# Kernel tuning notes

Measured on AMD Instinct MI355X. Metric: run time of the kernel, lower is better.

## Reference

```python
import jax, jax.numpy as jnp
import numpy as np

# DeformConv (v1, mmcv-style) config
N, C, H, W = 4, 64, 128, 128
OUT_C, KH, KW = 64, 3, 3
STRIDE, PAD, DIL, DG = 1, 1, 1, 1  # groups = 1


def setup_inputs() -> dict:
    key = jax.random.key(0)
    k1, k2, k3 = jax.random.split(key, 3)
    x = jax.random.normal(k1, (N, C, H, W), dtype=jnp.float32)
    offset = jax.random.normal(k2, (N, 2 * DG * KH * KW, H, W), dtype=jnp.float32)
    n_fan = C * KH * KW
    std = 1.0 / np.sqrt(n_fan)
    weight = jax.random.uniform(k3, (OUT_C, C, KH, KW), minval=-std, maxval=std, dtype=jnp.float32)
    return {"input_tensor": x, "offset": offset, "weight": weight}


def _deform_conv(x, offset, weight, stride, padding, dilation, dg):
    n, c, h, w = x.shape
    o, cin_g, kh, kw = weight.shape
    k = kh * kw
    ho = (h + 2 * padding - dilation * (kh - 1) - 1) // stride + 1
    wo = (w + 2 * padding - dilation * (kw - 1) - 1) // stride + 1

    # offset layout: [n, dg*k*2, ho, wo] with (dy, dx) pairs per kernel point
    off = offset.reshape(n, dg, k, 2, ho, wo)
    dy, dx = off[:, :, :, 0], off[:, :, :, 1]  # [n, dg, k, ho, wo]

    ky, kx = jnp.meshgrid(jnp.arange(kh), jnp.arange(kw), indexing="ij")
    ky = ky.reshape(k).astype(x.dtype)
    kx = kx.reshape(k).astype(x.dtype)

    base_y = (jnp.arange(ho) * stride - padding).astype(x.dtype)
    base_x = (jnp.arange(wo) * stride - padding).astype(x.dtype)
    # sampling positions [n, dg, k, ho, wo]
    py = base_y[None, None, None, :, None] + (ky * dilation)[None, None, :, None, None] + dy
    px = base_x[None, None, None, None, :] + (kx * dilation)[None, None, :, None, None] + dx

    cg = c // dg
    xg = x.reshape(n, dg, cg, h * w)

    y0 = jnp.floor(py)
    x0 = jnp.floor(px)
    ly = py - y0  # bilinear weights
    lx = px - x0
    y0i = y0.astype(jnp.int32)
    x0i = x0.astype(jnp.int32)

    def gather(yi, xi):
        # zero contribution for out-of-bounds neighbors (matches mmcv bilinear)
        valid = (yi >= 0) & (yi < h) & (xi >= 0) & (xi < w)
        idx = jnp.clip(yi, 0, h - 1) * w + jnp.clip(xi, 0, w - 1)  # [n, dg, k, ho, wo]
        v = jnp.take_along_axis(xg, idx.reshape(n, dg, 1, -1), axis=3)  # [n, dg, cg, k*ho*wo]
        v = v.reshape(n, dg, cg, k, ho, wo)
        return v * valid[:, :, None].astype(x.dtype)

    v00 = gather(y0i, x0i)
    v01 = gather(y0i, x0i + 1)
    v10 = gather(y0i + 1, x0i)
    v11 = gather(y0i + 1, x0i + 1)

    wy = ly[:, :, None]  # [n, dg, 1, k, ho, wo]
    wx = lx[:, :, None]
    sampled = (v00 * (1 - wy) * (1 - wx) + v01 * (1 - wy) * wx
               + v10 * wy * (1 - wx) + v11 * wy * wx)
    sampled = sampled.reshape(n, c, k, ho, wo)  # dg*cg == c, groups == 1

    return jnp.einsum("nckhw,ock->nohw", sampled, weight.reshape(o, cin_g, k))


def reference(input_tensor, offset, weight):
    return _deform_conv(input_tensor, offset, weight, STRIDE, PAD, DIL, DG)
```

## Files before the change

### kernel.cpp

```cpp
#include <hip/hip_runtime.h>

#define HW 16384
#define CIN 64
#define COUT 64
#define HH 128
#define WW 128
#define NB 4
#define PXB 32
#define TPB 4

typedef __attribute__((ext_vector_type(8))) short bf16x8;
typedef __attribute__((ext_vector_type(4))) float f32x4;
typedef __attribute__((ext_vector_type(8))) unsigned short u16x8;

__device__ __forceinline__ unsigned short f32_bf16(float f) {
  unsigned u = __builtin_bit_cast(unsigned, f);
  u += 0x7fffu + ((u >> 16) & 1u);
  return (unsigned short)(u >> 16);
}
__device__ __forceinline__ float bits_f32(unsigned u) {
  return __builtin_bit_cast(float, u);
}

#define SYNCB()                                              \
  do {                                                       \
    asm volatile("s_waitcnt lgkmcnt(0)" ::: "memory");       \
    __builtin_amdgcn_s_barrier();                            \
    __builtin_amdgcn_sched_barrier(0);                       \
  } while (0)

__global__ __launch_bounds__(256) void prep_kernel(
    const float* __restrict__ x, const float* __restrict__ w,
    unsigned short* __restrict__ xt, unsigned short* __restrict__ wt) {
  __shared__ float tile[64][65];
  const int bid = blockIdx.x;
  if (bid < 1024) {
    const int n = bid >> 8;
    const int hw0 = (bid & 255) * 64;
    const int tx = threadIdx.x & 63;
    const int ty = threadIdx.x >> 6;
    const float* xp = x + (size_t)n * CIN * HW;
    #pragma unroll
    for (int c = ty; c < 64; c += 4)
      tile[c][tx] = xp[(size_t)c * HW + hw0 + tx];
    __syncthreads();
    unsigned short* xtp = xt + (size_t)n * HW * CIN;
    #pragma unroll
    for (int hw = ty; hw < 64; hw += 4)
      xtp[(size_t)(hw0 + hw) * CIN + tx] = f32_bf16(tile[tx][hw]);
  } else {
    const int i = (bid - 1024) * 256 + threadIdx.x;
    if (i < 64 * 576) {
      const int o = i / 576;
      const int t = i % 576;
      const int c = t & 63;
      const int k = t >> 6;
      wt[i] = f32_bf16(w[((size_t)o * 64 + c) * 9 + k]);
    }
  }
}

__global__ __launch_bounds__(256, 2) void deform_mfma(
    const unsigned short* __restrict__ xt, const float* __restrict__ offset,
    const unsigned short* __restrict__ wt, float* __restrict__ out) {
  __shared__ unsigned short s[PXB][584];
  __shared__ f32x4 pw[288];
  __shared__ uint2 pidx[288];
  const int tid = threadIdx.x;
  const int wave = tid >> 6;
  const int lane = tid & 63;
  const int g16 = lane >> 4;
  const int li16 = lane & 15;
  const int px = wave * 8 + (lane >> 3);
  const int li8 = lane & 7;
  const int base = blockIdx.x * (PXB * TPB);
  const int n = base >> 14;
  const int rem_base = base & 16383;

  const float* offb = offset + (size_t)n * 18 * HW;
  const unsigned short* xli = xt + (size_t)n * HW * CIN + li8 * 8;

  const int px0 = tid & 31;
  const int tap0 = tid >> 5;

  bf16x8 bv[18];
  {
    const unsigned short* bp = wt + ((size_t)(wave * 16 + li16)) * 576 + g16 * 8;
    #pragma unroll
    for (int i = 0; i < 18; ++i)
      bv[i] = *(const bf16x8*)(bp + i * 32);
  }

  #define PARAMS(tt, tapv, dyv, dxv)                                       \
    do {                                                                   \
      const int rem = rem_base + (tt) * PXB + px0;                         \
      const int y = rem >> 7;                                              \
      const int x = rem & 127;                                             \
      const float fy = floorf(dyv);                                        \
      const float fx = floorf(dxv);                                        \
      const float ly = (dyv)-fy;                                           \
      const float lx = (dxv)-fx;                                           \
      const int y0 = y - 1 + ((tapv) / 3) + (int)fy;                       \
      const int x0 = x - 1 + ((tapv) % 3) + (int)fx;                       \
      const int y1 = y0 + 1, x1 = x0 + 1;                                  \
      const bool vy0 = (unsigned)y0 < (unsigned)HH;                        \
      const bool vy1 = (unsigned)y1 < (unsigned)HH;                        \
      const bool vx0 = (unsigned)x0 < (unsigned)WW;                        \
      const bool vx1 = (unsigned)x1 < (unsigned)WW;                        \
      const int cy0 = min(max(y0, 0), HH - 1);                             \
      const int cy1 = min(max(y1, 0), HH - 1);                             \
      const int cx0 = min(max(x0, 0), WW - 1);                             \
      const int cx1 = min(max(x1, 0), WW - 1);                             \
      const float omly = 1.f - ly, omlx = 1.f - lx;                        \
      f32x4 w4;                                                            \
      w4[0] = (vy0 && vx0) ? omly * omlx : 0.f;                            \
      w4[1] = (vy0 && vx1) ? omly * lx : 0.f;                              \
      w4[2] = (vy1 && vx0) ? ly * omlx : 0.f;                              \
      w4[3] = (vy1 && vx1) ? ly * lx : 0.f;                                \
      const unsigned i00 = (unsigned)(cy0 * WW + cx0);                     \
      const unsigned i01 = (unsigned)(cy0 * WW + cx1);                     \
      const unsigned i10 = (unsigned)(cy1 * WW + cx0);                     \
      const unsigned i11 = (unsigned)(cy1 * WW + cx1);                     \
      pw[(tapv)*32 + px0] = w4;                                            \
      pidx[(tapv)*32 + px0] = make_uint2(i00 | (i01 << 16), i10 | (i11 << 16)); \
    } while (0)

  u16x8 V[3][4];

  #define ISSUE(kk, sl)                                                    \
    do {                                                                   \
      const uint2 id = pidx[(kk)*32 + px];                                 \
      V[sl][0] = *(const u16x8*)(xli + (size_t)(id.x & 0xffffu) * CIN);    \
      V[sl][1] = *(const u16x8*)(xli + (size_t)(id.x >> 16) * CIN);        \
      V[sl][2] = *(const u16x8*)(xli + (size_t)(id.y & 0xffffu) * CIN);    \
      V[sl][3] = *(const u16x8*)(xli + (size_t)(id.y >> 16) * CIN);        \
    } while (0)

  #define BLEND(kk, sl)                                                    \
    do {                                                                   \
      const f32x4 w = pw[(kk)*32 + px];                                    \
      float a[8] = {0.f, 0.f, 0.f, 0.f, 0.f, 0.f, 0.f, 0.f};               \
      _Pragma("unroll")                                                    \
      for (int c = 0; c < 4; ++c) {                                        \
        _Pragma("unroll")                                                  \
        for (int j = 0; j < 8; ++j)                                        \
          a[j] = fmaf(bits_f32((unsigned)V[sl][c][j] << 16), w[c], a[j]);  \
      }                                                                    \
      unsigned r0, r1, r2, r3;                                             \
      asm("v_cvt_pk_bf16_f32 %0, %1, %2" : "=v"(r0) : "v"(a[0]), "v"(a[1])); \
      asm("v_cvt_pk_bf16_f32 %0, %1, %2" : "=v"(r1) : "v"(a[2]), "v"(a[3])); \
      asm("v_cvt_pk_bf16_f32 %0, %1, %2" : "=v"(r2) : "v"(a[4]), "v"(a[5])); \
      asm("v_cvt_pk_bf16_f32 %0, %1, %2" : "=v"(r3) : "v"(a[6]), "v"(a[7])); \
      *(uint4*)&s[px][(kk)*64 + li8 * 8] = make_uint4(r0, r1, r2, r3);     \
    } while (0)

  #define MFMA_OUT(remt)                                                   \
    do {                                                                   \
      f32x4 acc0 = {0.f, 0.f, 0.f, 0.f};                                   \
      f32x4 acc1 = {0.f, 0.f, 0.f, 0.f};                                   \
      const unsigned short* ap0 = &s[li16][g16 * 8];                       \
      const unsigned short* ap1 = &s[16 + li16][g16 * 8];                  \
      _Pragma("unroll")                                                    \
      for (int i = 0; i < 18; ++i) {                                       \
        bf16x8 a0 = *(const bf16x8*)(ap0 + i * 32);                        \
        bf16x8 a1 = *(const bf16x8*)(ap1 + i * 32);                        \
        acc0 = __builtin_amdgcn_mfma_f32_16x16x32_bf16(a0, bv[i], acc0, 0, 0, 0); \
        acc1 = __builtin_amdgcn_mfma_f32_16x16x32_bf16(a1, bv[i], acc1, 0, 0, 0); \
      }                                                                    \
      const int oc = wave * 16 + li16;                                     \
      float* ob = out + ((size_t)n * COUT + oc) * HW + (remt) + g16 * 4;   \
      *(f32x4*)ob = acc0;                                                  \
      *(f32x4*)(ob + 16) = acc1;                                           \
    } while (0)

  float dy0, dx0, dy1 = 0.f, dx1 = 0.f;
  {
    const int rem = rem_base + px0;
    dy0 = offb[(size_t)(2 * tap0) * HW + rem];
    dx0 = offb[(size_t)(2 * tap0 + 1) * HW + rem];
    if (tid < 32) {
      dy1 = offb[(size_t)16 * HW + rem];
      dx1 = offb[(size_t)17 * HW + rem];
    }
  }

  int prev_rem0 = 0;

  #pragma unroll 1
  for (int t = 0; t < TPB; ++t) {
    const int rem0 = rem_base + t * PXB;

    PARAMS(t, tap0, dy0, dx0);
    if (tid < 32) PARAMS(t, 8, dy1, dx1);
    SYNCB();

    if (t + 1 < TPB) {
      const int rem = rem_base + (t + 1) * PXB + px0;
      dy0 = offb[(size_t)(2 * tap0) * HW + rem];
      dx0 = offb[(size_t)(2 * tap0 + 1) * HW + rem];
      if (tid < 32) {
        dy1 = offb[(size_t)16 * HW + rem];
        dx1 = offb[(size_t)17 * HW + rem];
      }
    }

    ISSUE(0, 0);
    ISSUE(1, 1);
    ISSUE(2, 2);
    __builtin_amdgcn_sched_barrier(0);

    if (t > 0) MFMA_OUT(prev_rem0);
    SYNCB();

    BLEND(0, 0); ISSUE(3, 0);
    BLEND(1, 1); ISSUE(4, 1);
    BLEND(2, 2); ISSUE(5, 2);
    BLEND(3, 0); ISSUE(6, 0);
    BLEND(4, 1); ISSUE(7, 1);
    BLEND(5, 2); ISSUE(8, 2);
    BLEND(6, 0);
    BLEND(7, 1);
    BLEND(8, 2);
    SYNCB();

    prev_rem0 = rem0;
  }

  MFMA_OUT(prev_rem0);

  #undef PARAMS
  #undef ISSUE
  #undef BLEND
  #undef MFMA_OUT
}

__global__ __launch_bounds__(256) void deform_fallback(
    const float* __restrict__ xsrc, const float* __restrict__ offset,
    const float* __restrict__ wsrc, float* __restrict__ out) {
  __shared__ float s[16][576];
  const int wave = threadIdx.x >> 6;
  const int lane = threadIdx.x & 63;
  const int p0 = blockIdx.x * 16;
  for (int i = 0; i < 4; ++i) {
    const int p = p0 + wave * 4 + i;
    const int n = p >> 14;
    const int rem = p & 16383;
    const int y = rem >> 7;
    const int x = rem & 127;
    const float* off = offset + (size_t)n * 18 * HW + rem;
    const float* xb = xsrc + (size_t)n * CIN * HW;
    #pragma unroll
    for (int k = 0; k < 9; ++k) {
      const float dy = off[(size_t)(2 * k) * HW];
      const float dx = off[(size_t)(2 * k + 1) * HW];
      const float py = (float)(y - 1 + k / 3) + dy;
      const float px = (float)(x - 1 + k % 3) + dx;
      const float y0f = floorf(py), x0f = floorf(px);
      const float ly = py - y0f, lx = px - x0f;
      const int y0 = (int)y0f, x0 = (int)x0f;
      const int y1 = y0 + 1, x1 = x0 + 1;
      const bool vy0 = (y0 >= 0) && (y0 < HH), vy1 = (y1 >= 0) && (y1 < HH);
      const bool vx0 = (x0 >= 0) && (x0 < WW), vx1 = (x1 >= 0) && (x1 < WW);
      const int cy0 = min(max(y0, 0), HH - 1), cy1 = min(max(y1, 0), HH - 1);
      const int cx0 = min(max(x0, 0), WW - 1), cx1 = min(max(x1, 0), WW - 1);
      const float v00 = (vy0 && vx0) ? xb[(size_t)lane * HW + cy0 * WW + cx0] : 0.f;
      const float v01 = (vy0 && vx1) ? xb[(size_t)lane * HW + cy0 * WW + cx1] : 0.f;
      const float v10 = (vy1 && vx0) ? xb[(size_t)lane * HW + cy1 * WW + cx0] : 0.f;
      const float v11 = (vy1 && vx1) ? xb[(size_t)lane * HW + cy1 * WW + cx1] : 0.f;
      s[wave * 4 + i][k * 64 + lane] =
          v00 * (1.f - ly) * (1.f - lx) + v01 * (1.f - ly) * lx +
          v10 * ly * (1.f - lx) + v11 * ly * lx;
    }
  }
  __syncthreads();
  float a0 = 0.f, a1 = 0.f, a2 = 0.f, a3 = 0.f;
  const int pb = wave * 4;
  for (int t = 0; t < 576; ++t) {
    const int c = t & 63;
    const int k = t >> 6;
    const float wv = wsrc[((size_t)lane * 64 + c) * 9 + k];
    a0 += s[pb + 0][t] * wv;
    a1 += s[pb + 1][t] * wv;
    a2 += s[pb + 2][t] * wv;
    a3 += s[pb + 3][t] * wv;
  }
  const float acc[4] = {a0, a1, a2, a3};
  for (int i = 0; i < 4; ++i) {
    const int p = p0 + pb + i;
    const int n = p >> 14;
    const int rem = p & 16383;
    out[((size_t)n * COUT + lane) * HW + rem] = acc[i];
  }
}

extern "C" void kernel_launch(void* const* d_in, const int* in_sizes, int n_in,
                              void* d_out, int out_size, void* d_ws,
                              size_t ws_size, hipStream_t stream) {
  const float* x = (const float*)d_in[0];
  const float* offset = (const float*)d_in[1];
  const float* weight = (const float*)d_in[2];
  float* out = (float*)d_out;

  const size_t xt_elems = (size_t)NB * HW * CIN;
  const size_t wt_elems = (size_t)64 * 576;
  const size_t need = (xt_elems + wt_elems) * sizeof(short);

  if (ws_size >= need) {
    unsigned short* xtp = (unsigned short*)d_ws;
    unsigned short* wtp = xtp + xt_elems;
    prep_kernel<<<1024 + 144, 256, 0, stream>>>(x, weight, xtp, wtp);
    deform_mfma<<<NB * HW / (PXB * TPB), 256, 0, stream>>>(xtp, offset, wtp, out);
  } else {
    deform_fallback<<<NB * HW / 16, 256, 0, stream>>>(x, offset, weight, out);
  }
}
```

Before: 36.27 us.

## Double-buffer sampling params and deepen gather prefetch to four taps

Sampling weights and indices now live in double-buffered shared arrays. The next tile's params are computed at the end of the current blend phase, which removes one block barrier per iteration. The gather register ring grows from three slots to four, so more global loads are in flight during blending. This costs extra shared memory and more vector registers, which may hurt occupancy under the two-blocks-per-CU launch bound.

```diff
diff --git a/kernel.cpp b/kernel.cpp
--- a/kernel.cpp
+++ b/kernel.cpp
@@ -64,8 +64,8 @@
     const unsigned short* __restrict__ xt, const float* __restrict__ offset,
     const unsigned short* __restrict__ wt, float* __restrict__ out) {
   __shared__ unsigned short s[PXB][584];
-  __shared__ f32x4 pw[288];
-  __shared__ uint2 pidx[288];
+  __shared__ f32x4 pw[2][288];
+  __shared__ uint2 pidx[2][288];
   const int tid = threadIdx.x;
   const int wave = tid >> 6;
   const int lane = tid & 63;
@@ -91,7 +91,7 @@
       bv[i] = *(const bf16x8*)(bp + i * 32);
   }
 
-  #define PARAMS(tt, tapv, dyv, dxv)                                       \
+  #define PARAMS(tt, wb, tapv, dyv, dxv)                                   \
     do {                                                                   \
       const int rem = rem_base + (tt) * PXB + px0;                         \
       const int y = rem >> 7;                                              \
@@ -121,24 +121,25 @@
       const unsigned i01 = (unsigned)(cy0 * WW + cx1);                     \
       const unsigned i10 = (unsigned)(cy1 * WW + cx0);                     \
       const unsigned i11 = (unsigned)(cy1 * WW + cx1);                     \
-      pw[(tapv)*32 + px0] = w4;                                            \
-      pidx[(tapv)*32 + px0] = make_uint2(i00 | (i01 << 16), i10 | (i11 << 16)); \
+      pw[wb][(tapv)*32 + px0] = w4;                                        \
+      pidx[wb][(tapv)*32 + px0] =                                          \
+          make_uint2(i00 | (i01 << 16), i10 | (i11 << 16));                \
     } while (0)
 
-  u16x8 V[3][4];
-
-  #define ISSUE(kk, sl)                                                    \
+  u16x8 V[4][4];
+
+  #define ISSUE(kk, sl, rb)                                                \
     do {                                                                   \
-      const uint2 id = pidx[(kk)*32 + px];                                 \
+      const uint2 id = pidx[rb][(kk)*32 + px];                             \
       V[sl][0] = *(const u16x8*)(xli + (size_t)(id.x & 0xffffu) * CIN);    \
       V[sl][1] = *(const u16x8*)(xli + (size_t)(id.x >> 16) * CIN);        \
       V[sl][2] = *(const u16x8*)(xli + (size_t)(id.y & 0xffffu) * CIN);    \
       V[sl][3] = *(const u16x8*)(xli + (size_t)(id.y >> 16) * CIN);        \
     } while (0)
 
-  #define BLEND(kk, sl)                                                    \
+  #define BLEND(kk, sl, rb)                                                \
     do {                                                                   \
-      const f32x4 w = pw[(kk)*32 + px];                                    \
+      const f32x4 w = pw[rb][(kk)*32 + px];                                \
       float a[8] = {0.f, 0.f, 0.f, 0.f, 0.f, 0.f, 0.f, 0.f};               \
       _Pragma("unroll")                                                    \
       for (int c = 0; c < 4; ++c) {                                        \
@@ -183,16 +184,16 @@
       dx1 = offb[(size_t)17 * HW + rem];
     }
   }
+  PARAMS(0, 0, tap0, dy0, dx0);
+  if (tid < 32) PARAMS(0, 0, 8, dy1, dx1);
+  SYNCB();
 
   int prev_rem0 = 0;
 
   #pragma unroll 1
   for (int t = 0; t < TPB; ++t) {
     const int rem0 = rem_base + t * PXB;
-
-    PARAMS(t, tap0, dy0, dx0);
-    if (tid < 32) PARAMS(t, 8, dy1, dx1);
-    SYNCB();
+    const int rb = t & 1;
 
     if (t + 1 < TPB) {
       const int rem = rem_base + (t + 1) * PXB + px0;
@@ -204,23 +205,28 @@
       }
     }
 
-    ISSUE(0, 0);
-    ISSUE(1, 1);
-    ISSUE(2, 2);
+    ISSUE(0, 0, rb);
+    ISSUE(1, 1, rb);
+    ISSUE(2, 2, rb);
+    ISSUE(3, 3, rb);
     __builtin_amdgcn_sched_barrier(0);
 
     if (t > 0) MFMA_OUT(prev_rem0);
     SYNCB();
 
-    BLEND(0, 0); ISSUE(3, 0);
-    BLEND(1, 1); ISSUE(4, 1);
-    BLEND(2, 2); ISSUE(5, 2);
-    BLEND(3, 0); ISSUE(6, 0);
-    BLEND(4, 1); ISSUE(7, 1);
-    BLEND(5, 2); ISSUE(8, 2);
-    BLEND(6, 0);
-    BLEND(7, 1);
-    BLEND(8, 2);
+    BLEND(0, 0, rb); ISSUE(4, 0, rb);
+    BLEND(1, 1, rb); ISSUE(5, 1, rb);
+    BLEND(2, 2, rb); ISSUE(6, 2, rb);
+    BLEND(3, 3, rb); ISSUE(7, 3, rb);
+    BLEND(4, 0, rb); ISSUE(8, 0, rb);
+    BLEND(5, 1, rb);
+    BLEND(6, 2, rb);
+    BLEND(7, 3, rb);
+    BLEND(8, 0, rb);
+    if (t + 1 < TPB) {
+      PARAMS(t + 1, (t + 1) & 1, tap0, dy0, dx0);
+      if (tid < 32) PARAMS(t + 1, (t + 1) & 1, 8, dy1, dx1);
+    }
     SYNCB();
 
     prev_rem0 = rem0;
```

Result: no change. 36.07 us (-0.6%).
